# Optimization experiments

Hardware: AMD Instinct MI355X
Metric: run time of the kernel (lower is better)

Reference implementation:

```python
import jax, jax.numpy as jnp
import numpy as np

D_MODEL = 1024
N_HEADS = 16
D_HEAD = D_MODEL // N_HEADS  # 64
NUM_MEM_KV = 4
SCALE = D_HEAD ** -0.5


def setup_inputs() -> dict:
    key = jax.random.key(0)
    k1, k2, k3, k4 = jax.random.split(key, 4)
    x = jax.random.normal(k1, (4, 4096, D_MODEL), dtype=jnp.float32)
    mask = jax.random.randint(k2, (4, 4096), 0, 2).astype(jnp.int32)
    w_qkv = jax.random.normal(k3, (3 * D_MODEL, D_MODEL), dtype=jnp.float32) * 0.02
    mem_kv = jax.random.normal(k4, (2, N_HEADS, NUM_MEM_KV, D_HEAD), dtype=jnp.float32)
    return {"x": x, "w_qkv": w_qkv, "mem_kv": mem_kv, "mask": mask}


def reference(x, w_qkv, mem_kv, mask):
    b, l, _ = x.shape
    # qkv projection: nn.Linear applies x @ W^T; reshape matches torch view(..., h, d_head, 3)
    qkv = jnp.einsum('bld,ed->ble', x, w_qkv).reshape(b, l, N_HEADS, D_HEAD, 3)
    qkv = jnp.moveaxis(qkv, 2, 1)  # (b, h, l, d_head, 3)
    q, k, v = qkv[..., 0], qkv[..., 1], qkv[..., 2]

    m = mask.astype(x.dtype)[:, None, :, None]  # (b, 1, l, 1) per prepare_mask
    k = jnp.where(m == 0, -jnp.inf, k * m)

    # prepend learned memory kv along the sequence axis
    mk = jnp.broadcast_to(mem_kv[0], (b, N_HEADS, NUM_MEM_KV, D_HEAD))
    mv = jnp.broadcast_to(mem_kv[1], (b, N_HEADS, NUM_MEM_KV, D_HEAD))
    k = jnp.concatenate([mk, k], axis=-2)  # (b, h, m+l, d_head)
    v = jnp.concatenate([mv, v], axis=-2)

    q = jax.nn.softmax(q * SCALE, axis=-1)   # softmax over feature dim
    k = jax.nn.softmax(k, axis=-2)           # softmax over sequence dim; -inf rows -> 0 weight

    context = jnp.einsum('bhnd,bhne->bhde', k, v)   # (b, h, d_head, d_head)
    out = jnp.einsum('bhld,bhde->bhle', q, context)  # (b, h, l, d_head)
    out = out * m
    out = jnp.moveaxis(out, 1, 2).reshape(b, l, N_HEADS * D_HEAD)
    return out
```

## Files before the change

kernel.cpp:

```cpp
#include <hip/hip_runtime.h>

typedef _Float16 h8 __attribute__((ext_vector_type(8)));
typedef _Float16 h4 __attribute__((ext_vector_type(4)));
typedef float f4 __attribute__((ext_vector_type(4)));

typedef __attribute__((address_space(1))) const void GV;
typedef __attribute__((address_space(3))) void SV;

__device__ __forceinline__ void async16(const void* g, void* s) {
  __builtin_amdgcn_global_load_lds((GV*)g, (SV*)s, 16, 0, 0);
}


#define XC 2097152
#define WC 393216

__global__ __launch_bounds__(256) void cvt_f16(const float4* __restrict__ x,
                                               const float4* __restrict__ w,
                                               h8* __restrict__ xh,
                                               h8* __restrict__ wh) {
  int t = blockIdx.x * 256 + threadIdx.x;
  if (t < XC) {
    const int row = t >> 7, c7 = t & 127;
    const int dst = (row << 7) | (c7 & 120) | ((c7 & 7) ^ (row & 7));
    float4 a = x[t * 2], b = x[t * 2 + 1];
    h8 o = {(_Float16)a.x, (_Float16)a.y, (_Float16)a.z, (_Float16)a.w,
            (_Float16)b.x, (_Float16)b.y, (_Float16)b.z, (_Float16)b.w};
    xh[dst] = o;
  } else {
    const int u = t - XC;
    const int rp = u >> 7, c7 = u & 127;
    int sr;
    if (rp < 2048) {
      int h = rp >> 7, c = rp & 127;
      sr = h * 192 + ((c < 64) ? (c * 3 + 1) : ((c - 64) * 3 + 2));
    } else {
      int q = rp - 2048;
      sr = (q >> 6) * 192 + (q & 63) * 3;
    }
    const int dst = (rp << 7) | (c7 & 120) | ((c7 & 7) ^ (rp & 7));
    float4 a = w[sr * 256 + c7 * 2], b = w[sr * 256 + c7 * 2 + 1];
    h8 o = {(_Float16)a.x, (_Float16)a.y, (_Float16)a.z, (_Float16)a.w,
            (_Float16)b.x, (_Float16)b.y, (_Float16)b.z, (_Float16)b.w};
    wh[dst] = o;
  }
}

__global__ __launch_bounds__(256, 3) void gemm_fused(const _Float16* __restrict__ A,
                                                     const _Float16* __restrict__ W,
                                                     const int* __restrict__ mask,
                                                     _Float16* __restrict__ P,
                                                     float* __restrict__ part) {
  __shared__ _Float16 smem[128 * 128];
  _Float16* const As = smem;
  _Float16* const Bs = smem + 8192;
  const int tid = threadIdx.x;
  const int lane = tid & 63, wid = tid >> 6;
  const int wm = wid & 1, wn = wid >> 1;
  const int l15 = lane & 15, quad = lane >> 4;
  const int m0 = blockIdx.y * 128;
  const int n0 = blockIdx.x * 128;

  const f4 z = {0.f, 0.f, 0.f, 0.f};
  f4 acc[4][4];
#pragma unroll
  for (int i = 0; i < 4; ++i)
#pragma unroll
    for (int j = 0; j < 4; ++j) acc[i][j] = z;

  const int swz = l15 & 7;

  for (int kt = 0; kt < 16; ++kt) {
    const int k0 = kt * 64;
#pragma unroll
    for (int it = 0; it < 4; ++it) {
      const int idx = it * 256 + tid;
      const int row = idx >> 3, cg = idx & 7;
      async16(A + ((size_t)(m0 + row) * 1024 + k0 + cg * 8), As + idx * 8);
      async16(W + ((size_t)(n0 + row) * 1024 + k0 + cg * 8), Bs + idx * 8);
    }
    __syncthreads();
#pragma unroll
    for (int ks = 0; ks < 2; ++ks) {
      const int pc = ((ks << 2) | quad) ^ swz;
      h8 af[4], bf[4];
#pragma unroll
      for (int i = 0; i < 4; ++i)
        af[i] = *(const h8*)&As[(wm * 64 + i * 16 + l15) * 64 + pc * 8];
#pragma unroll
      for (int j = 0; j < 4; ++j)
        bf[j] = *(const h8*)&Bs[(wn * 64 + j * 16 + l15) * 64 + pc * 8];
#pragma unroll
      for (int i = 0; i < 4; ++i)
#pragma unroll
        for (int j = 0; j < 4; ++j)
          acc[i][j] = __builtin_amdgcn_mfma_f32_16x16x32_f16(af[i], bf[j], acc[i][j], 0, 0, 0);
    }
    __syncthreads();
  }

  if (n0 < 2048) {
    const int h = n0 >> 7;
    const int b = m0 >> 12;
    const int lc = (m0 & 4095) >> 7;
    const int bh = b * 16 + h;
#pragma unroll
    for (int i = 0; i < 4; ++i) {
      const int nb = wm * 64 + i * 16 + quad * 4;
#pragma unroll
      for (int j = 0; j < 4; ++j) {
        const int c = wn * 64 + j * 16 + l15;
        h4 o;
        if (wn == 0) {
#pragma unroll
          for (int r = 0; r < 4; ++r)
            o[r] = (_Float16)(mask[m0 + nb + r] ? __expf(acc[i][j][r]) : 0.f);
        } else {
#pragma unroll
          for (int r = 0; r < 4; ++r) o[r] = (_Float16)acc[i][j][r];
        }
        *(h4*)&smem[c * 128 + (nb ^ (l15 * 8))] = o;
      }
    }
    __syncthreads();
    f4 cacc[5];
#pragma unroll
    for (int i = 0; i < 5; ++i) cacc[i] = z;
    h8 bones;
    {
      const _Float16 o1 = (l15 == 0) ? (_Float16)1.f : (_Float16)0.f;
#pragma unroll
      for (int j = 0; j < 8; ++j) bones[j] = o1;
    }
    const int ds = wid * 16;
#pragma unroll
    for (int ks = 0; ks < 4; ++ks) {
      const int nb2 = (ks * 32 + quad * 8) ^ (l15 * 8);
      h8 a = *(const h8*)&smem[(ds + l15) * 128 + nb2];
#pragma unroll
      for (int et = 0; et < 4; ++et) {
        h8 bv = *(const h8*)&smem[(64 + et * 16 + l15) * 128 + nb2];
        cacc[et] = __builtin_amdgcn_mfma_f32_16x16x32_f16(a, bv, cacc[et], 0, 0, 0);
      }
      cacc[4] = __builtin_amdgcn_mfma_f32_16x16x32_f16(a, bones, cacc[4], 0, 0, 0);
    }
    const size_t pb = ((size_t)bh * 32 + lc) * 4160;
    const int dw = ds + quad * 4;
#pragma unroll
    for (int et = 0; et < 4; ++et)
#pragma unroll
      for (int r = 0; r < 4; ++r)
        part[pb + (size_t)(dw + r) * 64 + et * 16 + l15] = cacc[et][r];
    if (l15 == 0) {
#pragma unroll
      for (int r = 0; r < 4; ++r) part[pb + 4096 + dw + r] = cacc[4][r];
    }
  } else {
#pragma unroll
    for (int i = 0; i < 4; ++i) {
      const int rg = m0 + wm * 64 + i * 16 + quad * 4;
#pragma unroll
      for (int j = 0; j < 4; ++j) {
        const int qc = (n0 - 2048) + wn * 64 + j * 16 + l15;
#pragma unroll
        for (int r = 0; r < 4; ++r)
          P[(size_t)(rg + r) * 1024 + qc] = (_Float16)__expf(acc[i][j][r] * 0.125f);
      }
    }
  }
}

__global__ __launch_bounds__(256) void reduce_ctx(const float* __restrict__ part,
                                                  const float* __restrict__ memkv,
                                                  _Float16* __restrict__ ctxt) {
  const int bh = blockIdx.x;
  const int dsl = blockIdx.y;
  const int h = bh & 15;
  const int tid = threadIdx.x;
  const int dl = tid >> 6, e = tid & 63;
  const int d = dsl * 4 + dl;
  const size_t pb = (size_t)bh * 32 * 4160;

  float den = 0.f;
#pragma unroll 8
  for (int c = 0; c < 32; ++c) den += part[pb + (size_t)c * 4160 + 4096 + d];
  float s = 0.f;
#pragma unroll 8
  for (int c = 0; c < 32; ++c) s += part[pb + (size_t)c * 4160 + (size_t)d * 64 + e];
#pragma unroll
  for (int j = 0; j < 4; ++j) {
    const float ek = __expf(memkv[(h * 4 + j) * 64 + d]);
    den += ek;
    s += ek * memkv[4096 + (h * 4 + j) * 64 + e];
  }
  ctxt[(size_t)bh * 4096 + (size_t)e * 64 + d] = (_Float16)(s / den);
}

__global__ __launch_bounds__(256) void attn_out(const _Float16* __restrict__ P,
                                                const _Float16* __restrict__ ctxt,
                                                const int* __restrict__ mask,
                                                float* __restrict__ out) {
  const int l0 = blockIdx.x * 128;
  const int h = blockIdx.y;
  const int bh = (l0 >> 12) * 16 + h;
  const int tid = threadIdx.x;
  const int lane = tid & 63, wid = tid >> 6;
  const int l15 = lane & 15, quad = lane >> 4;

  h8 af[2][2], bf[2][4], bones;
  {
    const _Float16 o1 = (l15 == 0) ? (_Float16)1.f : (_Float16)0.f;
#pragma unroll
    for (int j = 0; j < 8; ++j) bones[j] = o1;
  }
#pragma unroll
  for (int i = 0; i < 2; ++i)
#pragma unroll
    for (int ks = 0; ks < 2; ++ks)
      af[i][ks] = *(const h8*)&P[(size_t)(l0 + wid * 32 + i * 16 + l15) * 1024 +
                                 h * 64 + ks * 32 + quad * 8];
#pragma unroll
  for (int ks = 0; ks < 2; ++ks)
#pragma unroll
    for (int et = 0; et < 4; ++et)
      bf[ks][et] = *(const h8*)&ctxt[(size_t)bh * 4096 +
                                     (size_t)(et * 16 + l15) * 64 + ks * 32 + quad * 8];

  const f4 z = {0.f, 0.f, 0.f, 0.f};
  f4 acc[2][5];
#pragma unroll
  for (int i = 0; i < 2; ++i)
#pragma unroll
    for (int j = 0; j < 5; ++j) acc[i][j] = z;
#pragma unroll
  for (int i = 0; i < 2; ++i)
#pragma unroll
    for (int ks = 0; ks < 2; ++ks) {
#pragma unroll
      for (int et = 0; et < 4; ++et)
        acc[i][et] = __builtin_amdgcn_mfma_f32_16x16x32_f16(af[i][ks], bf[ks][et], acc[i][et], 0, 0, 0);
      acc[i][4] = __builtin_amdgcn_mfma_f32_16x16x32_f16(af[i][ks], bones, acc[i][4], 0, 0, 0);
    }

#pragma unroll
  for (int i = 0; i < 2; ++i) {
#pragma unroll
    for (int r = 0; r < 4; ++r) {
      const int row = l0 + wid * 32 + i * 16 + quad * 4 + r;
      const float sb = __shfl(acc[i][4][r], lane & 48);
      const float iv = mask[row] ? 1.0f / sb : 0.0f;
#pragma unroll
      for (int et = 0; et < 4; ++et)
        out[(size_t)row * 1024 + h * 64 + et * 16 + l15] = acc[i][et][r] * iv;
    }
  }
}

extern "C" void kernel_launch(void* const* d_in, const int* in_sizes, int n_in,
                              void* d_out, int out_size, void* d_ws, size_t ws_size,
                              hipStream_t stream) {
  const float* x = (const float*)d_in[0];
  const float* w = (const float*)d_in[1];
  const float* memkv = (const float*)d_in[2];
  const int* mask = (const int*)d_in[3];
  float* out = (float*)d_out;

  char* ws = (char*)d_ws;
  _Float16* xh   = (_Float16*)(ws + 0);
  _Float16* wh   = (_Float16*)(ws + 33554432);
  _Float16* P    = (_Float16*)(ws + 39845888);
  float*    part = (float*)(ws + 73400320);
  _Float16* ctxt = (_Float16*)(ws + 107479040);

  cvt_f16<<<dim3(9728), dim3(256), 0, stream>>>((const float4*)x, (const float4*)w,
                                                (h8*)xh, (h8*)wh);
  gemm_fused<<<dim3(24, 128), dim3(256), 0, stream>>>(xh, wh, mask, P, part);
  reduce_ctx<<<dim3(64, 16), dim3(256), 0, stream>>>(part, memkv, ctxt);
  attn_out<<<dim3(128, 16), dim3(256), 0, stream>>>(P, ctxt, mask, out);
}
```

Measured before the change: 267.0 us.

## Enlarge GEMM tile to 256x256 with 8 waves and double-buffered async LDS pipeline

Expands the fused QKV GEMM block tile from 128x128 with 4 waves to 256x256 with 8 waves. The K loop now double-buffers LDS and issues async global-to-LDS loads for the next tiles between MFMA quarter-steps, using explicit barriers, waitcnt and setprio to overlap memory with compute. The epilogue is reworked so each block covers two heads, which halves the number of partial context chunks that reduce_ctx sums. It trades fewer blocks (768, which may underfill the machine's CUs) and 128KB of LDS per block for more data reuse per tile and hidden load latency.

```diff
diff --git a/kernel.cpp b/kernel.cpp
--- a/kernel.cpp
+++ b/kernel.cpp
@@ -46,80 +46,178 @@
   }
 }
 
-__global__ __launch_bounds__(256, 3) void gemm_fused(const _Float16* __restrict__ A,
+
+__device__ __forceinline__ void ld4(h8 (&dst)[2][4], const _Float16* buf, int rbase,
+                                    int l15, int quad, int swz) {
+#pragma unroll
+  for (int ks = 0; ks < 2; ++ks) {
+    const int pc = ((((ks << 2) | quad) ^ swz)) << 3;
+#pragma unroll
+    for (int i = 0; i < 4; ++i)
+      dst[ks][i] = *(const h8*)&buf[(rbase + i * 16 + l15) * 64 + pc];
+  }
+}
+
+__device__ __forceinline__ void ld2(h8 (&dst)[2][2], const _Float16* buf, int rbase,
+                                    int l15, int quad, int swz) {
+#pragma unroll
+  for (int ks = 0; ks < 2; ++ks) {
+    const int pc = ((((ks << 2) | quad) ^ swz)) << 3;
+#pragma unroll
+    for (int j = 0; j < 2; ++j)
+      dst[ks][j] = *(const h8*)&buf[(rbase + j * 16 + l15) * 64 + pc];
+  }
+}
+
+template <int MH, int NH>
+__device__ __forceinline__ void mq(f4 (&acc)[8][4], const h8 (&af)[2][4],
+                                   const h8 (&bf)[2][2]) {
+#pragma unroll
+  for (int ks = 0; ks < 2; ++ks)
+#pragma unroll
+    for (int i = 0; i < 4; ++i)
+#pragma unroll
+      for (int j = 0; j < 2; ++j)
+        acc[MH * 4 + i][NH * 2 + j] = __builtin_amdgcn_mfma_f32_16x16x32_f16(
+            af[ks][i], bf[ks][j], acc[MH * 4 + i][NH * 2 + j], 0, 0, 0);
+}
+
+__device__ __forceinline__ void stage(const _Float16* g, _Float16* l, int it, int tid) {
+  async16(g + (size_t)it * 65536, l + (it * 512 + tid) * 8);
+}
+
+__global__ __launch_bounds__(512, 2) void gemm_fused(const _Float16* __restrict__ A,
                                                      const _Float16* __restrict__ W,
                                                      const int* __restrict__ mask,
                                                      _Float16* __restrict__ P,
                                                      float* __restrict__ part) {
-  __shared__ _Float16 smem[128 * 128];
-  _Float16* const As = smem;
-  _Float16* const Bs = smem + 8192;
+  __shared__ _Float16 smem[65536];
+  _Float16* const As0 = smem;
+  _Float16* const As1 = smem + 16384;
+  _Float16* const Bs0 = smem + 32768;
+  _Float16* const Bs1 = smem + 49152;
   const int tid = threadIdx.x;
   const int lane = tid & 63, wid = tid >> 6;
   const int wm = wid & 1, wn = wid >> 1;
   const int l15 = lane & 15, quad = lane >> 4;
-  const int m0 = blockIdx.y * 128;
-  const int n0 = blockIdx.x * 128;
+  const int m0 = blockIdx.y * 256;
+  const int n0 = blockIdx.x * 256;
+  const int swz = l15 & 7;
+
+  const int r0 = tid >> 3, cg = tid & 7;
+  const _Float16* const Ab = A + (size_t)(m0 + r0) * 1024 + cg * 8;
+  const _Float16* const Bb = W + (size_t)(n0 + r0) * 1024 + cg * 8;
 
   const f4 z = {0.f, 0.f, 0.f, 0.f};
-  f4 acc[4][4];
-#pragma unroll
-  for (int i = 0; i < 4; ++i)
+  f4 acc[8][4];
+#pragma unroll
+  for (int i = 0; i < 8; ++i)
 #pragma unroll
     for (int j = 0; j < 4; ++j) acc[i][j] = z;
 
-  const int swz = l15 & 7;
-
+#pragma unroll
+  for (int it = 0; it < 4; ++it) {
+    stage(Ab, As0, it, tid);
+    stage(Bb, Bs0, it, tid);
+  }
+  stage(Ab + 64, As1, 0, tid);
+  stage(Bb + 64, Bs1, 0, tid);
+  stage(Ab + 64, As1, 1, tid);
+  stage(Bb + 64, Bs1, 1, tid);
+  asm volatile("s_waitcnt vmcnt(4)" ::: "memory");
+  __builtin_amdgcn_s_barrier();
+
+#pragma unroll 2
   for (int kt = 0; kt < 16; ++kt) {
-    const int k0 = kt * 64;
-#pragma unroll
-    for (int it = 0; it < 4; ++it) {
-      const int idx = it * 256 + tid;
-      const int row = idx >> 3, cg = idx & 7;
-      async16(A + ((size_t)(m0 + row) * 1024 + k0 + cg * 8), As + idx * 8);
-      async16(W + ((size_t)(n0 + row) * 1024 + k0 + cg * 8), Bs + idx * 8);
-    }
-    __syncthreads();
-#pragma unroll
-    for (int ks = 0; ks < 2; ++ks) {
-      const int pc = ((ks << 2) | quad) ^ swz;
-      h8 af[4], bf[4];
-#pragma unroll
-      for (int i = 0; i < 4; ++i)
-        af[i] = *(const h8*)&As[(wm * 64 + i * 16 + l15) * 64 + pc * 8];
-#pragma unroll
-      for (int j = 0; j < 4; ++j)
-        bf[j] = *(const h8*)&Bs[(wn * 64 + j * 16 + l15) * 64 + pc * 8];
-#pragma unroll
-      for (int i = 0; i < 4; ++i)
-#pragma unroll
-        for (int j = 0; j < 4; ++j)
-          acc[i][j] = __builtin_amdgcn_mfma_f32_16x16x32_f16(af[i], bf[j], acc[i][j], 0, 0, 0);
-    }
-    __syncthreads();
+    _Float16* const Ac = (kt & 1) ? As1 : As0;
+    _Float16* const Bc = (kt & 1) ? Bs1 : Bs0;
+    _Float16* const An = (kt & 1) ? As0 : As1;
+    _Float16* const Bn = (kt & 1) ? Bs0 : Bs1;
+    const _Float16* const Anx = Ab + (kt + 1) * 64;
+    const _Float16* const Bnx = Bb + (kt + 1) * 64;
+    h8 af[2][4], bf0[2][2], bf1[2][2];
+    const int arb = wm * 128, brb = wn * 64;
+
+    ld4(af, Ac, arb, l15, quad, swz);
+    ld2(bf0, Bc, brb, l15, quad, swz);
+    __builtin_amdgcn_s_barrier();
+    asm volatile("s_waitcnt lgkmcnt(0)" ::: "memory");
+    __builtin_amdgcn_s_setprio(1);
+    mq<0, 0>(acc, af, bf0);
+    __builtin_amdgcn_s_setprio(0);
+    __builtin_amdgcn_s_barrier();
+
+    ld2(bf1, Bc, brb + 32, l15, quad, swz);
+    if (kt < 15) {
+      stage(Anx, An, 2, tid);
+      stage(Bnx, Bn, 2, tid);
+    }
+    __builtin_amdgcn_s_barrier();
+    asm volatile("s_waitcnt lgkmcnt(0)" ::: "memory");
+    __builtin_amdgcn_s_setprio(1);
+    mq<0, 1>(acc, af, bf1);
+    __builtin_amdgcn_s_setprio(0);
+    __builtin_amdgcn_s_barrier();
+
+    ld4(af, Ac, arb + 64, l15, quad, swz);
+    __builtin_amdgcn_s_barrier();
+    asm volatile("s_waitcnt lgkmcnt(0)" ::: "memory");
+    __builtin_amdgcn_s_setprio(1);
+    mq<1, 0>(acc, af, bf0);
+    __builtin_amdgcn_s_setprio(0);
+    __builtin_amdgcn_s_barrier();
+
+    if (kt < 15) {
+      stage(Anx, An, 3, tid);
+      stage(Bnx, Bn, 3, tid);
+    }
+    __builtin_amdgcn_s_barrier();
+    __builtin_amdgcn_s_setprio(1);
+    mq<1, 1>(acc, af, bf1);
+    __builtin_amdgcn_s_setprio(0);
+    __builtin_amdgcn_s_barrier();
+
+    if (kt < 14) {
+      const _Float16* const A2 = Ab + (kt + 2) * 64;
+      const _Float16* const B2 = Bb + (kt + 2) * 64;
+      stage(A2, Ac, 0, tid);
+      stage(B2, Bc, 0, tid);
+      stage(A2, Ac, 1, tid);
+      stage(B2, Bc, 1, tid);
+      asm volatile("s_waitcnt vmcnt(4)" ::: "memory");
+      __builtin_amdgcn_s_barrier();
+    } else if (kt == 14) {
+      asm volatile("s_waitcnt vmcnt(0)" ::: "memory");
+      __builtin_amdgcn_s_barrier();
+    }
   }
 
   if (n0 < 2048) {
-    const int h = n0 >> 7;
+    const int h0 = n0 >> 7;
     const int b = m0 >> 12;
-    const int lc = (m0 & 4095) >> 7;
-    const int bh = b * 16 + h;
-#pragma unroll
-    for (int i = 0; i < 4; ++i) {
-      const int nb = wm * 64 + i * 16 + quad * 4;
+    const int lc = (m0 & 4095) >> 8;
+    const int hh = wn >> 1, isv = wn & 1;
+#pragma unroll
+    for (int i = 0; i < 8; ++i) {
+      const int nb = wm * 128 + i * 16 + quad * 4;
+      int mk[4];
+      if (isv == 0) {
+#pragma unroll
+        for (int r = 0; r < 4; ++r) mk[r] = mask[m0 + nb + r];
+      }
 #pragma unroll
       for (int j = 0; j < 4; ++j) {
-        const int c = wn * 64 + j * 16 + l15;
+        const int cw = isv * 64 + j * 16 + l15;
         h4 o;
-        if (wn == 0) {
+        if (isv == 0) {
 #pragma unroll
           for (int r = 0; r < 4; ++r)
-            o[r] = (_Float16)(mask[m0 + nb + r] ? __expf(acc[i][j][r]) : 0.f);
+            o[r] = (_Float16)(mk[r] ? __expf(acc[i][j][r]) : 0.f);
         } else {
 #pragma unroll
           for (int r = 0; r < 4; ++r) o[r] = (_Float16)acc[i][j][r];
         }
-        *(h4*)&smem[c * 128 + (nb ^ (l15 * 8))] = o;
+        *(h4*)&smem[(hh * 128 + cw) * 256 + (nb ^ (l15 * 8))] = o;
       }
     }
     __syncthreads();
@@ -132,20 +230,22 @@
 #pragma unroll
       for (int j = 0; j < 8; ++j) bones[j] = o1;
     }
-    const int ds = wid * 16;
-#pragma unroll
-    for (int ks = 0; ks < 4; ++ks) {
+    const int hw = wid >> 2, dsw = (wid & 3) * 16;
+    const _Float16* const hb = &smem[hw * 128 * 256];
+#pragma unroll
+    for (int ks = 0; ks < 8; ++ks) {
       const int nb2 = (ks * 32 + quad * 8) ^ (l15 * 8);
-      h8 a = *(const h8*)&smem[(ds + l15) * 128 + nb2];
+      h8 a = *(const h8*)&hb[(dsw + l15) * 256 + nb2];
 #pragma unroll
       for (int et = 0; et < 4; ++et) {
-        h8 bv = *(const h8*)&smem[(64 + et * 16 + l15) * 128 + nb2];
+        h8 bv = *(const h8*)&hb[(64 + et * 16 + l15) * 256 + nb2];
         cacc[et] = __builtin_amdgcn_mfma_f32_16x16x32_f16(a, bv, cacc[et], 0, 0, 0);
       }
       cacc[4] = __builtin_amdgcn_mfma_f32_16x16x32_f16(a, bones, cacc[4], 0, 0, 0);
     }
-    const size_t pb = ((size_t)bh * 32 + lc) * 4160;
-    const int dw = ds + quad * 4;
+    const int bh = b * 16 + h0 + hw;
+    const size_t pb = ((size_t)bh * 16 + lc) * 4160;
+    const int dw = dsw + quad * 4;
 #pragma unroll
     for (int et = 0; et < 4; ++et)
 #pragma unroll
@@ -156,12 +256,13 @@
       for (int r = 0; r < 4; ++r) part[pb + 4096 + dw + r] = cacc[4][r];
     }
   } else {
-#pragma unroll
-    for (int i = 0; i < 4; ++i) {
-      const int rg = m0 + wm * 64 + i * 16 + quad * 4;
+    const int q0 = (n0 - 2048) + wn * 64;
+#pragma unroll
+    for (int i = 0; i < 8; ++i) {
+      const int rg = m0 + wm * 128 + i * 16 + quad * 4;
 #pragma unroll
       for (int j = 0; j < 4; ++j) {
-        const int qc = (n0 - 2048) + wn * 64 + j * 16 + l15;
+        const int qc = q0 + j * 16 + l15;
 #pragma unroll
         for (int r = 0; r < 4; ++r)
           P[(size_t)(rg + r) * 1024 + qc] = (_Float16)__expf(acc[i][j][r] * 0.125f);
@@ -179,14 +280,14 @@
   const int tid = threadIdx.x;
   const int dl = tid >> 6, e = tid & 63;
   const int d = dsl * 4 + dl;
-  const size_t pb = (size_t)bh * 32 * 4160;
+  const size_t pb = (size_t)bh * 16 * 4160;
 
   float den = 0.f;
 #pragma unroll 8
-  for (int c = 0; c < 32; ++c) den += part[pb + (size_t)c * 4160 + 4096 + d];
+  for (int c = 0; c < 16; ++c) den += part[pb + (size_t)c * 4160 + 4096 + d];
   float s = 0.f;
 #pragma unroll 8
-  for (int c = 0; c < 32; ++c) s += part[pb + (size_t)c * 4160 + (size_t)d * 64 + e];
+  for (int c = 0; c < 16; ++c) s += part[pb + (size_t)c * 4160 + (size_t)d * 64 + e];
 #pragma unroll
   for (int j = 0; j < 4; ++j) {
     const float ek = __expf(memkv[(h * 4 + j) * 64 + d]);
@@ -274,7 +375,7 @@
 
   cvt_f16<<<dim3(9728), dim3(256), 0, stream>>>((const float4*)x, (const float4*)w,
                                                 (h8*)xh, (h8*)wh);
-  gemm_fused<<<dim3(24, 128), dim3(256), 0, stream>>>(xh, wh, mask, P, part);
+  gemm_fused<<<dim3(12, 64), dim3(512), 0, stream>>>(xh, wh, mask, P, part);
   reduce_ctx<<<dim3(64, 16), dim3(256), 0, stream>>>(part, memkv, ctxt);
   attn_out<<<dim3(128, 16), dim3(256), 0, stream>>>(P, ctxt, mask, out);
 }
```

Result: no change. 262.0 us (-1.9%).

## Fuse Q projection with context application to eliminate P intermediate

Applied to the files above, without the earlier changes.

Splits the fused GEMM so it computes only the K/V projection and context partials. The Q projection moves into a new kernel that also applies exp, multiplies by the reduced context in LDS and writes the output directly. This removes the global write and re-read of the 32 MB fp16 P tensor and one kernel launch. The cost is that the Q GEMM now runs after the context reduction instead of overlapping with the K/V work, with a smaller grid and a heavier epilogue per block.

```diff
diff --git a/kernel.cpp b/kernel.cpp
--- a/kernel.cpp
+++ b/kernel.cpp
@@ -13,7 +13,6 @@
 
 
 #define XC 2097152
-#define WC 393216
 
 __global__ __launch_bounds__(256) void cvt_f16(const float4* __restrict__ x,
                                                const float4* __restrict__ w,
@@ -46,11 +45,10 @@
   }
 }
 
-__global__ __launch_bounds__(256, 3) void gemm_fused(const _Float16* __restrict__ A,
-                                                     const _Float16* __restrict__ W,
-                                                     const int* __restrict__ mask,
-                                                     _Float16* __restrict__ P,
-                                                     float* __restrict__ part) {
+__global__ __launch_bounds__(256, 3) void kv_gemm(const _Float16* __restrict__ A,
+                                                  const _Float16* __restrict__ W,
+                                                  const int* __restrict__ mask,
+                                                  float* __restrict__ part) {
   __shared__ _Float16 smem[128 * 128];
   _Float16* const As = smem;
   _Float16* const Bs = smem + 8192;
@@ -99,74 +97,60 @@
     __syncthreads();
   }
 
-  if (n0 < 2048) {
-    const int h = n0 >> 7;
-    const int b = m0 >> 12;
-    const int lc = (m0 & 4095) >> 7;
-    const int bh = b * 16 + h;
-#pragma unroll
-    for (int i = 0; i < 4; ++i) {
-      const int nb = wm * 64 + i * 16 + quad * 4;
-#pragma unroll
-      for (int j = 0; j < 4; ++j) {
-        const int c = wn * 64 + j * 16 + l15;
-        h4 o;
-        if (wn == 0) {
-#pragma unroll
-          for (int r = 0; r < 4; ++r)
-            o[r] = (_Float16)(mask[m0 + nb + r] ? __expf(acc[i][j][r]) : 0.f);
-        } else {
-#pragma unroll
-          for (int r = 0; r < 4; ++r) o[r] = (_Float16)acc[i][j][r];
-        }
-        *(h4*)&smem[c * 128 + (nb ^ (l15 * 8))] = o;
+  const int h = n0 >> 7;
+  const int b = m0 >> 12;
+  const int lc = (m0 & 4095) >> 7;
+  const int bh = b * 16 + h;
+#pragma unroll
+  for (int i = 0; i < 4; ++i) {
+    const int nb = wm * 64 + i * 16 + quad * 4;
+#pragma unroll
+    for (int j = 0; j < 4; ++j) {
+      const int c = wn * 64 + j * 16 + l15;
+      h4 o;
+      if (wn == 0) {
+#pragma unroll
+        for (int r = 0; r < 4; ++r)
+          o[r] = (_Float16)(mask[m0 + nb + r] ? __expf(acc[i][j][r]) : 0.f);
+      } else {
+#pragma unroll
+        for (int r = 0; r < 4; ++r) o[r] = (_Float16)acc[i][j][r];
       }
-    }
-    __syncthreads();
-    f4 cacc[5];
-#pragma unroll
-    for (int i = 0; i < 5; ++i) cacc[i] = z;
-    h8 bones;
-    {
-      const _Float16 o1 = (l15 == 0) ? (_Float16)1.f : (_Float16)0.f;
-#pragma unroll
-      for (int j = 0; j < 8; ++j) bones[j] = o1;
-    }
-    const int ds = wid * 16;
-#pragma unroll
-    for (int ks = 0; ks < 4; ++ks) {
-      const int nb2 = (ks * 32 + quad * 8) ^ (l15 * 8);
-      h8 a = *(const h8*)&smem[(ds + l15) * 128 + nb2];
-#pragma unroll
-      for (int et = 0; et < 4; ++et) {
-        h8 bv = *(const h8*)&smem[(64 + et * 16 + l15) * 128 + nb2];
-        cacc[et] = __builtin_amdgcn_mfma_f32_16x16x32_f16(a, bv, cacc[et], 0, 0, 0);
-      }
-      cacc[4] = __builtin_amdgcn_mfma_f32_16x16x32_f16(a, bones, cacc[4], 0, 0, 0);
-    }
-    const size_t pb = ((size_t)bh * 32 + lc) * 4160;
-    const int dw = ds + quad * 4;
-#pragma unroll
-    for (int et = 0; et < 4; ++et)
-#pragma unroll
-      for (int r = 0; r < 4; ++r)
-        part[pb + (size_t)(dw + r) * 64 + et * 16 + l15] = cacc[et][r];
-    if (l15 == 0) {
-#pragma unroll
-      for (int r = 0; r < 4; ++r) part[pb + 4096 + dw + r] = cacc[4][r];
-    }
-  } else {
-#pragma unroll
-    for (int i = 0; i < 4; ++i) {
-      const int rg = m0 + wm * 64 + i * 16 + quad * 4;
-#pragma unroll
-      for (int j = 0; j < 4; ++j) {
-        const int qc = (n0 - 2048) + wn * 64 + j * 16 + l15;
-#pragma unroll
-        for (int r = 0; r < 4; ++r)
-          P[(size_t)(rg + r) * 1024 + qc] = (_Float16)__expf(acc[i][j][r] * 0.125f);
-      }
-    }
+      *(h4*)&smem[c * 128 + (nb ^ (l15 * 8))] = o;
+    }
+  }
+  __syncthreads();
+  f4 cacc[5];
+#pragma unroll
+  for (int i = 0; i < 5; ++i) cacc[i] = z;
+  h8 bones;
+  {
+    const _Float16 o1 = (l15 == 0) ? (_Float16)1.f : (_Float16)0.f;
+#pragma unroll
+    for (int j = 0; j < 8; ++j) bones[j] = o1;
+  }
+  const int ds = wid * 16;
+#pragma unroll
+  for (int ks = 0; ks < 4; ++ks) {
+    const int nb2 = (ks * 32 + quad * 8) ^ (l15 * 8);
+    h8 a = *(const h8*)&smem[(ds + l15) * 128 + nb2];
+#pragma unroll
+    for (int et = 0; et < 4; ++et) {
+      h8 bv = *(const h8*)&smem[(64 + et * 16 + l15) * 128 + nb2];
+      cacc[et] = __builtin_amdgcn_mfma_f32_16x16x32_f16(a, bv, cacc[et], 0, 0, 0);
+    }
+    cacc[4] = __builtin_amdgcn_mfma_f32_16x16x32_f16(a, bones, cacc[4], 0, 0, 0);
+  }
+  const size_t pb = ((size_t)bh * 32 + lc) * 4160;
+  const int dw = ds + quad * 4;
+#pragma unroll
+  for (int et = 0; et < 4; ++et)
+#pragma unroll
+    for (int r = 0; r < 4; ++r)
+      part[pb + (size_t)(dw + r) * 64 + et * 16 + l15] = cacc[et][r];
+  if (l15 == 0) {
+#pragma unroll
+    for (int r = 0; r < 4; ++r) part[pb + 4096 + dw + r] = cacc[4][r];
   }
 }
 
@@ -196,62 +180,117 @@
   ctxt[(size_t)bh * 4096 + (size_t)e * 64 + d] = (_Float16)(s / den);
 }
 
-__global__ __launch_bounds__(256) void attn_out(const _Float16* __restrict__ P,
-                                                const _Float16* __restrict__ ctxt,
-                                                const int* __restrict__ mask,
-                                                float* __restrict__ out) {
-  const int l0 = blockIdx.x * 128;
-  const int h = blockIdx.y;
-  const int bh = (l0 >> 12) * 16 + h;
+__global__ __launch_bounds__(256, 3) void qpv(const _Float16* __restrict__ A,
+                                              const _Float16* __restrict__ W,
+                                              const _Float16* __restrict__ ctxt,
+                                              const int* __restrict__ mask,
+                                              float* __restrict__ out) {
+  __shared__ _Float16 smem[128 * 128];
+  _Float16* const As = smem;
+  _Float16* const Bs = smem + 8192;
   const int tid = threadIdx.x;
   const int lane = tid & 63, wid = tid >> 6;
+  const int wm = wid & 1, wn = wid >> 1;
   const int l15 = lane & 15, quad = lane >> 4;
-
-  h8 af[2][2], bf[2][4], bones;
+  const int m0 = blockIdx.y * 128;
+  const int n0 = blockIdx.x * 128;
+
+  const f4 z = {0.f, 0.f, 0.f, 0.f};
+  f4 acc[4][4];
+#pragma unroll
+  for (int i = 0; i < 4; ++i)
+#pragma unroll
+    for (int j = 0; j < 4; ++j) acc[i][j] = z;
+
+  const int swz = l15 & 7;
+
+  for (int kt = 0; kt < 16; ++kt) {
+    const int k0 = kt * 64;
+#pragma unroll
+    for (int it = 0; it < 4; ++it) {
+      const int idx = it * 256 + tid;
+      const int row = idx >> 3, cg = idx & 7;
+      async16(A + ((size_t)(m0 + row) * 1024 + k0 + cg * 8), As + idx * 8);
+      async16(W + ((size_t)(2048 + n0 + row) * 1024 + k0 + cg * 8), Bs + idx * 8);
+    }
+    __syncthreads();
+#pragma unroll
+    for (int ks = 0; ks < 2; ++ks) {
+      const int pc = ((ks << 2) | quad) ^ swz;
+      h8 af[4], bf[4];
+#pragma unroll
+      for (int i = 0; i < 4; ++i)
+        af[i] = *(const h8*)&As[(wm * 64 + i * 16 + l15) * 64 + pc * 8];
+#pragma unroll
+      for (int j = 0; j < 4; ++j)
+        bf[j] = *(const h8*)&Bs[(wn * 64 + j * 16 + l15) * 64 + pc * 8];
+#pragma unroll
+      for (int i = 0; i < 4; ++i)
+#pragma unroll
+        for (int j = 0; j < 4; ++j)
+          acc[i][j] = __builtin_amdgcn_mfma_f32_16x16x32_f16(bf[j], af[i], acc[i][j], 0, 0, 0);
+    }
+    __syncthreads();
+  }
+
+#pragma unroll
+  for (int i = 0; i < 4; ++i) {
+    const int m = wm * 64 + i * 16 + l15;
+    _Float16* const prow = &smem[m * 128 + wn * 64];
+#pragma unroll
+    for (int j = 0; j < 4; ++j) {
+      h4 o;
+#pragma unroll
+      for (int r = 0; r < 4; ++r) o[r] = (_Float16)__expf(acc[i][j][r] * 0.125f);
+      const int c3 = (j * 2 + (quad >> 1)) ^ (l15 & 7);
+      *(h4*)&prow[c3 * 8 + (quad & 1) * 4] = o;
+    }
+  }
+  __syncthreads();
+
+  const int hw = wid >> 1;
+  const int mb = (wid & 1) * 64;
+  const int h = (n0 >> 6) + hw;
+  const int bh = (m0 >> 12) * 16 + h;
+  f4 cacc[4][5];
+#pragma unroll
+  for (int i = 0; i < 4; ++i)
+#pragma unroll
+    for (int j = 0; j < 5; ++j) cacc[i][j] = z;
+  h8 bones;
   {
     const _Float16 o1 = (l15 == 0) ? (_Float16)1.f : (_Float16)0.f;
 #pragma unroll
     for (int j = 0; j < 8; ++j) bones[j] = o1;
   }
 #pragma unroll
-  for (int i = 0; i < 2; ++i)
-#pragma unroll
-    for (int ks = 0; ks < 2; ++ks)
-      af[i][ks] = *(const h8*)&P[(size_t)(l0 + wid * 32 + i * 16 + l15) * 1024 +
-                                 h * 64 + ks * 32 + quad * 8];
-#pragma unroll
-  for (int ks = 0; ks < 2; ++ks)
+  for (int ks = 0; ks < 2; ++ks) {
+    h8 bf[4];
 #pragma unroll
     for (int et = 0; et < 4; ++et)
-      bf[ks][et] = *(const h8*)&ctxt[(size_t)bh * 4096 +
-                                     (size_t)(et * 16 + l15) * 64 + ks * 32 + quad * 8];
-
-  const f4 z = {0.f, 0.f, 0.f, 0.f};
-  f4 acc[2][5];
-#pragma unroll
-  for (int i = 0; i < 2; ++i)
-#pragma unroll
-    for (int j = 0; j < 5; ++j) acc[i][j] = z;
-#pragma unroll
-  for (int i = 0; i < 2; ++i)
-#pragma unroll
-    for (int ks = 0; ks < 2; ++ks) {
+      bf[et] = *(const h8*)&ctxt[(size_t)bh * 4096 +
+                                 (size_t)(et * 16 + l15) * 64 + ks * 32 + quad * 8];
+#pragma unroll
+    for (int i2 = 0; i2 < 4; ++i2) {
+      const int m = mb + i2 * 16 + l15;
+      const int ch = ((ks * 4 + quad) ^ (l15 & 7)) * 8;
+      h8 a = *(const h8*)&smem[m * 128 + hw * 64 + ch];
 #pragma unroll
       for (int et = 0; et < 4; ++et)
-        acc[i][et] = __builtin_amdgcn_mfma_f32_16x16x32_f16(af[i][ks], bf[ks][et], acc[i][et], 0, 0, 0);
-      acc[i][4] = __builtin_amdgcn_mfma_f32_16x16x32_f16(af[i][ks], bones, acc[i][4], 0, 0, 0);
-    }
-
-#pragma unroll
-  for (int i = 0; i < 2; ++i) {
+        cacc[i2][et] = __builtin_amdgcn_mfma_f32_16x16x32_f16(a, bf[et], cacc[i2][et], 0, 0, 0);
+      cacc[i2][4] = __builtin_amdgcn_mfma_f32_16x16x32_f16(a, bones, cacc[i2][4], 0, 0, 0);
+    }
+  }
+#pragma unroll
+  for (int i2 = 0; i2 < 4; ++i2) {
 #pragma unroll
     for (int r = 0; r < 4; ++r) {
-      const int row = l0 + wid * 32 + i * 16 + quad * 4 + r;
-      const float sb = __shfl(acc[i][4][r], lane & 48);
+      const int row = m0 + mb + i2 * 16 + quad * 4 + r;
+      const float sb = __shfl(cacc[i2][4][r], lane & 48);
       const float iv = mask[row] ? 1.0f / sb : 0.0f;
 #pragma unroll
       for (int et = 0; et < 4; ++et)
-        out[(size_t)row * 1024 + h * 64 + et * 16 + l15] = acc[i][et][r] * iv;
+        out[(size_t)row * 1024 + h * 64 + et * 16 + l15] = cacc[i2][et][r] * iv;
     }
   }
 }
@@ -268,13 +307,12 @@
   char* ws = (char*)d_ws;
   _Float16* xh   = (_Float16*)(ws + 0);
   _Float16* wh   = (_Float16*)(ws + 33554432);
-  _Float16* P    = (_Float16*)(ws + 39845888);
-  float*    part = (float*)(ws + 73400320);
-  _Float16* ctxt = (_Float16*)(ws + 107479040);
+  float*    part = (float*)(ws + 39845888);
+  _Float16* ctxt = (_Float16*)(ws + 73924608);
 
   cvt_f16<<<dim3(9728), dim3(256), 0, stream>>>((const float4*)x, (const float4*)w,
                                                 (h8*)xh, (h8*)wh);
-  gemm_fused<<<dim3(24, 128), dim3(256), 0, stream>>>(xh, wh, mask, P, part);
+  kv_gemm<<<dim3(16, 128), dim3(256), 0, stream>>>(xh, wh, mask, part);
   reduce_ctx<<<dim3(64, 16), dim3(256), 0, stream>>>(part, memkv, ctxt);
-  attn_out<<<dim3(128, 16), dim3(256), 0, stream>>>(P, ctxt, mask, out);
-}
+  qpv<<<dim3(8, 128), dim3(256), 0, stream>>>(xh, wh, ctxt, mask, out);
+}
```

New measurement: 262.0 us. Within noise of the previous version (-1.9%).
